# Optimization experiments

Hardware: AMD Instinct MI355X
Metric: run time of the kernel (lower is better)

The kernel has to match this reference:

```python
import itertools
import jax, jax.numpy as jnp
import numpy as np

N_LEVELS = 16
N_FEATS = 2
LOG2_T = 19
BASE_RES = 16.0
FINEST_RES = 512.0
N_POINTS = 2 ** 21
MASK = np.uint32((1 << LOG2_T) - 1)
PRIMES = jnp.array([1, 2654435761, 805459861], dtype=jnp.uint32)
# 8 corner offsets of a voxel, [8, 3]
OFFSETS = jnp.array(list(itertools.product([0, 1], repeat=3)), dtype=jnp.int32)
BOX_MIN = jnp.zeros((3,), dtype=jnp.float32)
BOX_MAX = jnp.ones((3,), dtype=jnp.float32)
# per-level growth factor b = exp((log(finest)-log(base))/(L-1))
B_FACTOR = float(np.exp((np.log(FINEST_RES) - np.log(BASE_RES)) / (N_LEVELS - 1)))


def setup_inputs() -> dict:
    key = jax.random.key(0)
    k1, k2 = jax.random.split(key)
    x = jax.random.uniform(k1, (N_POINTS, 3), dtype=jnp.float32)
    # nn.init.uniform_(w, a=-1e-4, b=1e-4)
    tables = jax.random.uniform(k2, (N_LEVELS, 2 ** LOG2_T, N_FEATS),
                                dtype=jnp.float32, minval=-1e-4, maxval=1e-4)
    return {"x": x, "tables": tables}


def _hash(vidx):
    # vidx: [N, 8, 3] int32 voxel-corner integer coords
    v = vidx.astype(jnp.uint32)
    h = (v[..., 0] * PRIMES[0]) ^ (v[..., 1] * PRIMES[1]) ^ (v[..., 2] * PRIMES[2])
    return (h & MASK).astype(jnp.int32)  # [N, 8]


def _embed_level(x, table, resolution):
    # x: [N,3] float, table: [T,F], resolution: python float
    grid = (BOX_MAX - BOX_MIN) / resolution                      # [3]
    xc = jnp.clip(x, BOX_MIN, BOX_MAX)
    bl = jnp.floor((xc - BOX_MIN) / grid).astype(jnp.int32)      # [N,3]
    vmin = bl.astype(jnp.float32) * grid + BOX_MIN               # [N,3]
    vidx = bl[:, None, :] + OFFSETS[None, :, :]                  # [N,8,3]
    emb = table[_hash(vidx)]                                     # [N,8,F]
    rel = (xc - vmin) / grid                                     # [N,3]
    # trilinear weights: prod over dims of rel (offset=1) / 1-rel (offset=0)
    w = jnp.prod(jnp.where(OFFSETS[None, :, :] == 1,
                           rel[:, None, :], 1.0 - rel[:, None, :]), axis=-1)  # [N,8]
    return jnp.sum(w[..., None] * emb, axis=1)                   # [N,F]


def reference(x, tables):
    outs = []
    for i in range(N_LEVELS):
        resolution = float(np.floor(BASE_RES * B_FACTOR ** i))
        outs.append(_embed_level(x, tables[i], resolution))
    return jnp.concatenate(outs, axis=-1)  # [N, L*F]
```

## Files before the change

### kernel.cpp

```cpp
#include <hip/hip_runtime.h>
#include <stdint.h>


constexpr int kLevels = 16;
constexpr int kPoints = 1 << 21;
constexpr uint32_t kTableSize = 1u << 19;
constexpr uint32_t kMask = kTableSize - 1u;
constexpr size_t kPackedBytes = (size_t)kLevels * kTableSize * 4;
constexpr size_t kLvlOutBytes = (size_t)kLevels * kPoints * 4;

typedef float f32x4 __attribute__((ext_vector_type(4)));
typedef uint32_t u32x4 __attribute__((ext_vector_type(4)));

constexpr int kS0 = 17, kS1 = 21, kS2 = 26;
constexpr int kN0 = kS0 * kS0 * kS0;
constexpr int kN1 = kS1 * kS1 * kS1;
constexpr int kN2 = kS2 * kS2 * kS2;
constexpr int kB1 = kN0, kB2 = kN0 + kN1;
constexpr int kNDense = kN0 + kN1 + kN2;

constexpr int kV3n = 33 * 33 * 33;
constexpr int kV4n = 41 * 41 * 41;
constexpr int kV5n = 51 * 51 * 51;
constexpr int kV6n = 65 * 65 * 65;
constexpr int kVTot = kV3n + kV4n + kV5n + kV6n;
constexpr size_t kV3Base = 131072;
constexpr size_t kV4Base = kV3Base + (size_t)kV3n * 32;
constexpr size_t kV5Base = kV4Base + (size_t)kV4n * 32;
constexpr size_t kV6Base = kPackedBytes + (size_t)7 * kPoints * 4;

__constant__ float c_res[kLevels] = {
    16.f, 20.f, 25.f, 32.f, 40.f, 50.f, 64.f, 80.f,
    101.f, 128.f, 161.f, 203.f, 256.f, 322.f, 406.f, 512.f};

__device__ __forceinline__ uint32_t bf16_rtne_hi(float f) {
    uint32_t u = __float_as_uint(f);
    return (u + 0x7FFFu + ((u >> 16) & 1u)) >> 16;
}
__device__ __forceinline__ float bflo(uint32_t e) {
    return __uint_as_float(e << 16);
}
__device__ __forceinline__ float bfhi(uint32_t e) {
    return __uint_as_float(e & 0xFFFF0000u);
}

__global__ __launch_bounds__(256) void pack_tables_kernel(
    const float* __restrict__ tables, uint32_t* __restrict__ packed, int base)
{
    const int i = base + blockIdx.x * 256 + threadIdx.x;
    const f32x4 v = reinterpret_cast<const f32x4*>(tables)[i];
    uint2 o;
    o.x = bf16_rtne_hi(v.x) | (bf16_rtne_hi(v.y) << 16);
    o.y = bf16_rtne_hi(v.z) | (bf16_rtne_hi(v.w) << 16);
    reinterpret_cast<uint2*>(packed)[i] = o;
}

template <int S, int LVL>
__device__ __forceinline__ void build_dense_one(
    int r, const float* __restrict__ tables, uint32_t* __restrict__ dst)
{
    const int bz = r % S;
    const int t = r / S;
    const int by = t % S;
    const int bx = t / S;
    const uint32_t h = ((uint32_t)bx ^ ((uint32_t)by * 2654435761u) ^
                        ((uint32_t)bz * 805459861u)) & kMask;
    const float* src = tables + (((size_t)LVL << 19) + h) * 2;
    dst[r] = bf16_rtne_hi(src[0]) | (bf16_rtne_hi(src[1]) << 16);
}

__global__ __launch_bounds__(256) void build_dense012_kernel(
    const float* __restrict__ tables, uint32_t* __restrict__ dense)
{
    const int idx = blockIdx.x * 256 + threadIdx.x;
    if (idx >= kNDense) return;
    if (idx < kB1)      build_dense_one<kS0, 0>(idx,       tables, dense);
    else if (idx < kB2) build_dense_one<kS1, 1>(idx - kB1, tables, dense + kB1);
    else                build_dense_one<kS2, 2>(idx - kB2, tables, dense + kB2);
}

template <int S, int LVL>
__device__ __forceinline__ void build_vox_one(
    int v, const float* __restrict__ tables, u32x4* __restrict__ dst)
{
    const int bz = v % S;
    const int t = v / S;
    const int by = t % S;
    const int bx = t / S;
    const float* tab = tables + (((size_t)LVL << 19) * 2);
    uint32_t e[8];
#pragma unroll
    for (int c = 0; c < 8; ++c) {
        const uint32_t xx = (uint32_t)(bx + ((c >> 2) & 1));
        const uint32_t yy = (uint32_t)(by + ((c >> 1) & 1));
        const uint32_t zz = (uint32_t)(bz + (c & 1));
        const uint32_t h = (xx ^ (yy * 2654435761u) ^ (zz * 805459861u)) & kMask;
        const float* src = tab + (size_t)h * 2;
        e[c] = bf16_rtne_hi(src[0]) | (bf16_rtne_hi(src[1]) << 16);
    }
    u32x4 q0, q1;
    q0.x = e[0]; q0.y = e[1]; q0.z = e[2]; q0.w = e[3];
    q1.x = e[4]; q1.y = e[5]; q1.z = e[6]; q1.w = e[7];
    dst[2 * v + 0] = q0;
    dst[2 * v + 1] = q1;
}

__global__ __launch_bounds__(256) void build_vox_kernel(
    const float* __restrict__ tables, char* __restrict__ ws)
{
    const int v = blockIdx.x * 256 + threadIdx.x;
    if (v >= kVTot) return;
    if (v < kV3n)
        build_vox_one<33, 3>(v, tables, (u32x4*)(ws + kV3Base));
    else if (v < kV3n + kV4n)
        build_vox_one<41, 4>(v - kV3n, tables, (u32x4*)(ws + kV4Base));
    else if (v < kV3n + kV4n + kV5n)
        build_vox_one<51, 5>(v - kV3n - kV4n, tables, (u32x4*)(ws + kV5Base));
    else
        build_vox_one<65, 6>(v - kV3n - kV4n - kV5n, tables,
                             (u32x4*)(ws + kV6Base));
}

template <int S, int BASE, int LVL>
__device__ __forceinline__ void eval_coarse(
    const uint32_t* __restrict__ lds, float px, float py, float pz, float r,
    uint32_t* __restrict__ lvl_out, int n)
{
    const float tx = px * r, ty = py * r, tz = pz * r;
    const float fx = floorf(tx), fy = floorf(ty), fz = floorf(tz);
    const int bx = (int)fx, by = (int)fy, bz = (int)fz;
    const float rx = tx - fx, ry = ty - fy, rz = tz - fz;
    const int c = BASE + (bx * S + by) * S + bz;
    const uint32_t e000 = lds[c],             e001 = lds[c + 1];
    const uint32_t e010 = lds[c + S],         e011 = lds[c + S + 1];
    const uint32_t e100 = lds[c + S * S],     e101 = lds[c + S * S + 1];
    const uint32_t e110 = lds[c + S * S + S], e111 = lds[c + S * S + S + 1];
    const float wx1 = rx, wx0 = 1.f - rx;
    const float wy1 = ry, wy0 = 1.f - ry;
    const float wz1 = rz, wz0 = 1.f - rz;
    float a0 = 0.f, a1 = 0.f;
    a0 = fmaf(wx0 * wy0 * wz0, bflo(e000), a0);
    a1 = fmaf(wx0 * wy0 * wz0, bfhi(e000), a1);
    a0 = fmaf(wx0 * wy0 * wz1, bflo(e001), a0);
    a1 = fmaf(wx0 * wy0 * wz1, bfhi(e001), a1);
    a0 = fmaf(wx0 * wy1 * wz0, bflo(e010), a0);
    a1 = fmaf(wx0 * wy1 * wz0, bfhi(e010), a1);
    a0 = fmaf(wx0 * wy1 * wz1, bflo(e011), a0);
    a1 = fmaf(wx0 * wy1 * wz1, bfhi(e011), a1);
    a0 = fmaf(wx1 * wy0 * wz0, bflo(e100), a0);
    a1 = fmaf(wx1 * wy0 * wz0, bfhi(e100), a1);
    a0 = fmaf(wx1 * wy0 * wz1, bflo(e101), a0);
    a1 = fmaf(wx1 * wy0 * wz1, bfhi(e101), a1);
    a0 = fmaf(wx1 * wy1 * wz0, bflo(e110), a0);
    a1 = fmaf(wx1 * wy1 * wz0, bfhi(e110), a1);
    a0 = fmaf(wx1 * wy1 * wz1, bflo(e111), a0);
    a1 = fmaf(wx1 * wy1 * wz1, bfhi(e111), a1);
    lvl_out[(size_t)LVL * kPoints + n] =
        bf16_rtne_hi(a0) | (bf16_rtne_hi(a1) << 16);
}

__global__ __launch_bounds__(512) void coarse_kernel(
    const float* __restrict__ x, const uint32_t* __restrict__ dense,
    uint32_t* __restrict__ lvl_out)
{
    __shared__ uint32_t s_tab[kNDense];
    for (int i = threadIdx.x; i < kNDense; i += 512) s_tab[i] = dense[i];
    __syncthreads();

    const int n0 = blockIdx.x * 2048 + threadIdx.x;
#pragma unroll
    for (int k = 0; k < 4; ++k) {
        const int n = n0 + k * 512;
        const float px = fminf(fmaxf(x[3 * n + 0], 0.0f), 1.0f);
        const float py = fminf(fmaxf(x[3 * n + 1], 0.0f), 1.0f);
        const float pz = fminf(fmaxf(x[3 * n + 2], 0.0f), 1.0f);
        eval_coarse<kS0, 0,   0>(s_tab, px, py, pz, 16.f, lvl_out, n);
        eval_coarse<kS1, kB1, 1>(s_tab, px, py, pz, 20.f, lvl_out, n);
        eval_coarse<kS2, kB2, 2>(s_tab, px, py, pz, 25.f, lvl_out, n);
    }
}

template <int R, int LVL>
__device__ __forceinline__ void eval_vox(
    const u32x4* __restrict__ V, float px, float py, float pz,
    uint32_t* __restrict__ lvl_out, int n)
{
    const float r = (float)R;
    const float tx = px * r, ty = py * r, tz = pz * r;
    const float fx = floorf(tx), fy = floorf(ty), fz = floorf(tz);
    const int bx = (int)fx, by = (int)fy, bz = (int)fz;
    const float rx = tx - fx, ry = ty - fy, rz = tz - fz;
    constexpr int S = R + 1;
    const int idx = (bx * S + by) * S + bz;
    const u32x4 q0 = V[2 * idx + 0];
    const u32x4 q1 = V[2 * idx + 1];
    const float wx1 = rx, wx0 = 1.f - rx;
    const float wy1 = ry, wy0 = 1.f - ry;
    const float wz1 = rz, wz0 = 1.f - rz;
    float a0 = 0.f, a1 = 0.f;
    a0 = fmaf(wx0 * wy0 * wz0, bflo(q0.x), a0);
    a1 = fmaf(wx0 * wy0 * wz0, bfhi(q0.x), a1);
    a0 = fmaf(wx0 * wy0 * wz1, bflo(q0.y), a0);
    a1 = fmaf(wx0 * wy0 * wz1, bfhi(q0.y), a1);
    a0 = fmaf(wx0 * wy1 * wz0, bflo(q0.z), a0);
    a1 = fmaf(wx0 * wy1 * wz0, bfhi(q0.z), a1);
    a0 = fmaf(wx0 * wy1 * wz1, bflo(q0.w), a0);
    a1 = fmaf(wx0 * wy1 * wz1, bfhi(q0.w), a1);
    a0 = fmaf(wx1 * wy0 * wz0, bflo(q1.x), a0);
    a1 = fmaf(wx1 * wy0 * wz0, bfhi(q1.x), a1);
    a0 = fmaf(wx1 * wy0 * wz1, bflo(q1.y), a0);
    a1 = fmaf(wx1 * wy0 * wz1, bfhi(q1.y), a1);
    a0 = fmaf(wx1 * wy1 * wz0, bflo(q1.z), a0);
    a1 = fmaf(wx1 * wy1 * wz0, bfhi(q1.z), a1);
    a0 = fmaf(wx1 * wy1 * wz1, bflo(q1.w), a0);
    a1 = fmaf(wx1 * wy1 * wz1, bfhi(q1.w), a1);
    lvl_out[(size_t)LVL * kPoints + n] =
        bf16_rtne_hi(a0) | (bf16_rtne_hi(a1) << 16);
}

__global__ __launch_bounds__(256) void mid_kernel(
    const float* __restrict__ x, const char* __restrict__ ws,
    uint32_t* __restrict__ lvl_out)
{
    const int b = blockIdx.x;
    const int sub = b >> 11;
    const int chunk = b & 2047;
    const int n0 = chunk * 1024 + threadIdx.x;
#pragma unroll
    for (int k = 0; k < 4; ++k) {
        const int n = n0 + k * 256;
        const float px = fminf(fmaxf(x[3 * n + 0], 0.0f), 1.0f);
        const float py = fminf(fmaxf(x[3 * n + 1], 0.0f), 1.0f);
        const float pz = fminf(fmaxf(x[3 * n + 2], 0.0f), 1.0f);
        if (sub == 0)
            eval_vox<32, 3>((const u32x4*)(ws + kV3Base), px, py, pz, lvl_out, n);
        else if (sub == 1)
            eval_vox<40, 4>((const u32x4*)(ws + kV4Base), px, py, pz, lvl_out, n);
        else if (sub == 2)
            eval_vox<50, 5>((const u32x4*)(ws + kV5Base), px, py, pz, lvl_out, n);
        else
            eval_vox<64, 6>((const u32x4*)(ws + kV6Base), px, py, pz, lvl_out, n);
    }
}

struct PtSt {
    float rx, ry, rz;
    uint32_t sel;
    uint2 p0, p1, p2, p3;
};

__device__ __forceinline__ void issue_pt(
    PtSt& st, const float* __restrict__ x, int n, float r,
    const uint32_t* __restrict__ tab)
{
    const float px = fminf(fmaxf(x[3 * n + 0], 0.f), 1.f);
    const float py = fminf(fmaxf(x[3 * n + 1], 0.f), 1.f);
    const float pz = fminf(fmaxf(x[3 * n + 2], 0.f), 1.f);
    const float tx = px * r, ty = py * r, tz = pz * r;
    const float fx = floorf(tx), fy = floorf(ty), fz = floorf(tz);
    const int bx = (int)fx, by = (int)fy, bz = (int)fz;
    st.rx = tx - fx;  st.ry = ty - fy;  st.rz = tz - fz;
    const uint32_t hy0 = (uint32_t)by * 2654435761u;
    const uint32_t hy1 = (uint32_t)(by + 1) * 2654435761u;
    const uint32_t hz0 = (uint32_t)bz * 805459861u;
    const uint32_t hz1 = (uint32_t)(bz + 1) * 805459861u;
    const uint32_t bxu = (uint32_t)bx, bx1 = bxu + 1u;
    const uint32_t m0 = hy0 ^ hz0, m1 = hy0 ^ hz1;
    const uint32_t m2 = hy1 ^ hz0, m3 = hy1 ^ hz1;
    if ((bx & 1) == 0) {
        const uint32_t h0 = (bxu ^ m0) & kMask;
        const uint32_t h1 = (bxu ^ m1) & kMask;
        const uint32_t h2 = (bxu ^ m2) & kMask;
        const uint32_t h3 = (bxu ^ m3) & kMask;
        st.sel = (h0 & 1u) | ((h1 & 1u) << 1) |
                 ((h2 & 1u) << 2) | ((h3 & 1u) << 3);
        st.p0 = *reinterpret_cast<const uint2*>(tab + (h0 & ~1u));
        st.p1 = *reinterpret_cast<const uint2*>(tab + (h1 & ~1u));
        st.p2 = *reinterpret_cast<const uint2*>(tab + (h2 & ~1u));
        st.p3 = *reinterpret_cast<const uint2*>(tab + (h3 & ~1u));
    } else {
        st.sel = 0u;
        st.p0.x = tab[(bxu ^ m0) & kMask];  st.p0.y = tab[(bx1 ^ m0) & kMask];
        st.p1.x = tab[(bxu ^ m1) & kMask];  st.p1.y = tab[(bx1 ^ m1) & kMask];
        st.p2.x = tab[(bxu ^ m2) & kMask];  st.p2.y = tab[(bx1 ^ m2) & kMask];
        st.p3.x = tab[(bxu ^ m3) & kMask];  st.p3.y = tab[(bx1 ^ m3) & kMask];
    }
}

__device__ __forceinline__ void consume_pt(
    const PtSt& st, uint32_t* __restrict__ w, int n)
{
    const float wx1 = st.rx, wx0 = 1.f - st.rx;
    const float wy1 = st.ry, wy0 = 1.f - st.ry;
    const float wz1 = st.rz, wz0 = 1.f - st.rz;
    const float w0 = wy0 * wz0, w1 = wy0 * wz1;
    const float w2 = wy1 * wz0, w3 = wy1 * wz1;
    const uint32_t e0 = (st.sel & 1u) ? st.p0.y : st.p0.x;
    const uint32_t f0 = (st.sel & 1u) ? st.p0.x : st.p0.y;
    const uint32_t e1 = (st.sel & 2u) ? st.p1.y : st.p1.x;
    const uint32_t f1 = (st.sel & 2u) ? st.p1.x : st.p1.y;
    const uint32_t e2 = (st.sel & 4u) ? st.p2.y : st.p2.x;
    const uint32_t f2 = (st.sel & 4u) ? st.p2.x : st.p2.y;
    const uint32_t e3 = (st.sel & 8u) ? st.p3.y : st.p3.x;
    const uint32_t f3 = (st.sel & 8u) ? st.p3.x : st.p3.y;
    float a0 = 0.f, a1 = 0.f;
    a0 = fmaf(w0, fmaf(wx0, bflo(e0), wx1 * bflo(f0)), a0);
    a1 = fmaf(w0, fmaf(wx0, bfhi(e0), wx1 * bfhi(f0)), a1);
    a0 = fmaf(w1, fmaf(wx0, bflo(e1), wx1 * bflo(f1)), a0);
    a1 = fmaf(w1, fmaf(wx0, bfhi(e1), wx1 * bfhi(f1)), a1);
    a0 = fmaf(w2, fmaf(wx0, bflo(e2), wx1 * bflo(f2)), a0);
    a1 = fmaf(w2, fmaf(wx0, bfhi(e2), wx1 * bfhi(f2)), a1);
    a0 = fmaf(w3, fmaf(wx0, bflo(e3), wx1 * bflo(f3)), a0);
    a1 = fmaf(w3, fmaf(wx0, bfhi(e3), wx1 * bfhi(f3)), a1);
    w[n] = bf16_rtne_hi(a0) | (bf16_rtne_hi(a1) << 16);
}

__global__ __launch_bounds__(256) void fine_kernel(
    const float* __restrict__ x,
    const uint32_t* __restrict__ packed,
    uint32_t* __restrict__ lvl_out)
{
    const int b = blockIdx.x;
    const int level = 7 + (b >> 11);
    const int chunk = b & 2047;

    const float r = c_res[level];
    const uint32_t* __restrict__ tab = packed + (size_t)level * kTableSize;
    uint32_t* __restrict__ w = lvl_out + (size_t)level * kPoints;

    const int n0 = chunk * 1024 + threadIdx.x;

    PtSt A, B;
    issue_pt(A, x, n0 + 0 * 256, r, tab);
    issue_pt(B, x, n0 + 1 * 256, r, tab);
    __builtin_amdgcn_sched_barrier(0);
    consume_pt(A, w, n0 + 0 * 256);
    __builtin_amdgcn_sched_barrier(0);
    issue_pt(A, x, n0 + 2 * 256, r, tab);
    __builtin_amdgcn_sched_barrier(0);
    consume_pt(B, w, n0 + 1 * 256);
    __builtin_amdgcn_sched_barrier(0);
    issue_pt(B, x, n0 + 3 * 256, r, tab);
    __builtin_amdgcn_sched_barrier(0);
    consume_pt(A, w, n0 + 2 * 256);
    __builtin_amdgcn_sched_barrier(0);
    consume_pt(B, w, n0 + 3 * 256);
}

__global__ __launch_bounds__(256) void untile_kernel(
    const uint32_t* __restrict__ lvl_out, float* __restrict__ out)
{
    const int n = blockIdx.x * 256 + threadIdx.x;
    float vals[2 * kLevels];
#pragma unroll
    for (int l = 0; l < kLevels; ++l) {
        const uint32_t u = lvl_out[(size_t)l * kPoints + n];
        vals[2 * l + 0] = bflo(u);
        vals[2 * l + 1] = bfhi(u);
    }
    float4* o4 = reinterpret_cast<float4*>(out + (size_t)n * (2 * kLevels));
#pragma unroll
    for (int kq = 0; kq < 8; ++kq) {
        o4[kq] = make_float4(vals[4 * kq + 0], vals[4 * kq + 1],
                             vals[4 * kq + 2], vals[4 * kq + 3]);
    }
}

__device__ __forceinline__ void eval_level(
    float px, float py, float pz, float r,
    const uint32_t* __restrict__ tab, float& a0, float& a1)
{
    const float tx = px * r, ty = py * r, tz = pz * r;
    const float fx = floorf(tx), fy = floorf(ty), fz = floorf(tz);
    const int bx = (int)fx, by = (int)fy, bz = (int)fz;
    const float rx = tx - fx, ry = ty - fy, rz = tz - fz;

    const uint32_t hx0 = (uint32_t)bx;
    const uint32_t hx1 = (uint32_t)(bx + 1);
    const uint32_t hy0 = (uint32_t)by * 2654435761u;
    const uint32_t hy1 = (uint32_t)(by + 1) * 2654435761u;
    const uint32_t hz0 = (uint32_t)bz * 805459861u;
    const uint32_t hz1 = (uint32_t)(bz + 1) * 805459861u;

    const float wx1 = rx, wx0 = 1.0f - rx;
    const float wy1 = ry, wy0 = 1.0f - ry;
    const float wz1 = rz, wz0 = 1.0f - rz;

    a0 = 0.0f; a1 = 0.0f;
#pragma unroll
    for (int c = 0; c < 8; ++c) {
        const uint32_t h = (((c & 4) ? hx1 : hx0) ^
                            ((c & 2) ? hy1 : hy0) ^
                            ((c & 1) ? hz1 : hz0)) & kMask;
        const uint32_t e = tab[h];
        const float w = ((c & 4) ? wx1 : wx0) *
                        ((c & 2) ? wy1 : wy0) *
                        ((c & 1) ? wz1 : wz0);
        a0 = fmaf(w, bflo(e), a0);
        a1 = fmaf(w, bfhi(e), a1);
    }
}

__global__ __launch_bounds__(256) void direct_kernel(
    const float* __restrict__ x,
    const float* __restrict__ tables,
    float* __restrict__ out)
{
    const int n = blockIdx.x * 256 + threadIdx.x;
    float px = fminf(fmaxf(x[3 * n + 0], 0.0f), 1.0f);
    float py = fminf(fmaxf(x[3 * n + 1], 0.0f), 1.0f);
    float pz = fminf(fmaxf(x[3 * n + 2], 0.0f), 1.0f);

    const float res_tab[kLevels] = {
        16.f, 20.f, 25.f, 32.f, 40.f, 50.f, 64.f, 80.f,
        101.f, 128.f, 161.f, 203.f, 256.f, 322.f, 406.f, 512.f};

    float acc[2 * kLevels];
#pragma unroll
    for (int l = 0; l < kLevels; ++l) {
        const float r = res_tab[l];
        const float tx = px * r, ty = py * r, tz = pz * r;
        const float fx = floorf(tx), fy = floorf(ty), fz = floorf(tz);
        const int bx = (int)fx, by = (int)fy, bz = (int)fz;
        const float rx = tx - fx, ry = ty - fy, rz = tz - fz;
        const uint32_t hx0 = (uint32_t)bx;
        const uint32_t hx1 = (uint32_t)(bx + 1);
        const uint32_t hy0 = (uint32_t)by * 2654435761u;
        const uint32_t hy1 = (uint32_t)(by + 1) * 2654435761u;
        const uint32_t hz0 = (uint32_t)bz * 805459861u;
        const uint32_t hz1 = (uint32_t)(bz + 1) * 805459861u;
        const float wx1 = rx, wx0 = 1.0f - rx;
        const float wy1 = ry, wy0 = 1.0f - ry;
        const float wz1 = rz, wz0 = 1.0f - rz;
        const float2* __restrict__ tab =
            reinterpret_cast<const float2*>(tables) + (size_t)l * kTableSize;
        float a0 = 0.0f, a1 = 0.0f;
#pragma unroll
        for (int c = 0; c < 8; ++c) {
            const uint32_t h = (((c & 4) ? hx1 : hx0) ^
                                ((c & 2) ? hy1 : hy0) ^
                                ((c & 1) ? hz1 : hz0)) & kMask;
            const float2 e = tab[h];
            const float w = ((c & 4) ? wx1 : wx0) *
                            ((c & 2) ? wy1 : wy0) *
                            ((c & 1) ? wz1 : wz0);
            a0 = fmaf(w, e.x, a0);
            a1 = fmaf(w, e.y, a1);
        }
        acc[2 * l + 0] = a0;
        acc[2 * l + 1] = a1;
    }
    float4* o4 = reinterpret_cast<float4*>(out + (size_t)n * (2 * kLevels));
#pragma unroll
    for (int kq = 0; kq < 8; ++kq) {
        o4[kq] = make_float4(acc[4 * kq + 0], acc[4 * kq + 1],
                             acc[4 * kq + 2], acc[4 * kq + 3]);
    }
}

__global__ __launch_bounds__(256) void direct_packed_kernel(
    const float* __restrict__ x,
    const uint32_t* __restrict__ packed,
    float* __restrict__ out)
{
    const int n = blockIdx.x * 256 + threadIdx.x;
    float px = fminf(fmaxf(x[3 * n + 0], 0.0f), 1.0f);
    float py = fminf(fmaxf(x[3 * n + 1], 0.0f), 1.0f);
    float pz = fminf(fmaxf(x[3 * n + 2], 0.0f), 1.0f);

    const float res_tab[kLevels] = {
        16.f, 20.f, 25.f, 32.f, 40.f, 50.f, 64.f, 80.f,
        101.f, 128.f, 161.f, 203.f, 256.f, 322.f, 406.f, 512.f};

    float acc[2 * kLevels];
#pragma unroll
    for (int l = 0; l < kLevels; ++l) {
        float a0, a1;
        eval_level(px, py, pz, res_tab[l],
                   packed + (size_t)l * kTableSize, a0, a1);
        acc[2 * l + 0] = a0;
        acc[2 * l + 1] = a1;
    }
    float4* o4 = reinterpret_cast<float4*>(out + (size_t)n * (2 * kLevels));
#pragma unroll
    for (int kq = 0; kq < 8; ++kq) {
        o4[kq] = make_float4(acc[4 * kq + 0], acc[4 * kq + 1],
                             acc[4 * kq + 2], acc[4 * kq + 3]);
    }
}

extern "C" void kernel_launch(void* const* d_in, const int* in_sizes, int n_in,
                              void* d_out, int out_size, void* d_ws, size_t ws_size,
                              hipStream_t stream) {
    const float* x = (const float*)d_in[0];
    const float* tables = (const float*)d_in[1];
    float* out = (float*)d_out;

    if (ws_size >= kPackedBytes + kLvlOutBytes) {
        char* ws = (char*)d_ws;
        uint32_t* packed = (uint32_t*)ws;
        uint32_t* lvl_out = (uint32_t*)(ws + kPackedBytes);
        uint32_t* dense012 = (uint32_t*)ws;

        hipLaunchKernelGGL(pack_tables_kernel,
                           dim3((9 << 19) / 2 / 256), dim3(256),
                           0, stream, tables, packed, (7 << 19) / 2);
        hipLaunchKernelGGL(build_dense012_kernel,
                           dim3((kNDense + 255) / 256), dim3(256),
                           0, stream, tables, dense012);
        hipLaunchKernelGGL(build_vox_kernel,
                           dim3((kVTot + 255) / 256), dim3(256),
                           0, stream, tables, ws);
        hipLaunchKernelGGL(coarse_kernel, dim3(kPoints / 2048), dim3(512),
                           0, stream, x, dense012, lvl_out);
        hipLaunchKernelGGL(mid_kernel, dim3(4 * 2048), dim3(256),
                           0, stream, x, (const char*)ws, lvl_out);
        hipLaunchKernelGGL(fine_kernel, dim3(9 * 2048), dim3(256),
                           0, stream, x, packed, lvl_out);
        hipLaunchKernelGGL(untile_kernel, dim3(kPoints / 256), dim3(256),
                           0, stream, lvl_out, out);
    } else if (ws_size >= kPackedBytes) {
        uint32_t* packed = (uint32_t*)d_ws;
        hipLaunchKernelGGL(pack_tables_kernel,
                           dim3((kLevels * kTableSize / 2) / 256), dim3(256),
                           0, stream, tables, packed, 0);
        hipLaunchKernelGGL(direct_packed_kernel, dim3(kPoints / 256), dim3(256),
                           0, stream, x, packed, out);
    } else {
        hipLaunchKernelGGL(direct_kernel, dim3(kPoints / 256), dim3(256),
                           0, stream, x, tables, out);
    }
}
```

Before: 562.1 us.

## Build per-vertex dense grids before voxel tables and software-pipeline mid levels

The voxel tables for levels 3-6 are now built in two steps. A new kernel first gathers one hashed bf16 entry per grid vertex into a dense array. The voxel builder then reads its 8 corners from that dense array instead of recomputing 8 hashes and doing 8 random gathers per voxel. The mid kernel is restructured to load all point coordinates up front and interleave two in-flight voxel loads with the math, using sched_barriers for double-buffering. This adds an extra kernel launch and workspace region at hard-coded offsets, and uses float2 loads in the dense builder.

```diff
diff --git a/kernel.cpp b/kernel.cpp
--- a/kernel.cpp
+++ b/kernel.cpp
@@ -28,6 +28,10 @@
 constexpr size_t kV4Base = kV3Base + (size_t)kV3n * 32;
 constexpr size_t kV5Base = kV4Base + (size_t)kV4n * 32;
 constexpr size_t kV6Base = kPackedBytes + (size_t)7 * kPoints * 4;
+constexpr size_t kD3Base = 7731456;
+constexpr size_t kD4Base = 7875328;
+constexpr size_t kD5Base = 8151296;
+constexpr size_t kD6Base = 8681984;
 
 __constant__ float c_res[kLevels] = {
     16.f, 20.f, 25.f, 32.f, 40.f, 50.f, 64.f, 80.f,
@@ -65,8 +69,9 @@
     const int bx = t / S;
     const uint32_t h = ((uint32_t)bx ^ ((uint32_t)by * 2654435761u) ^
                         ((uint32_t)bz * 805459861u)) & kMask;
-    const float* src = tables + (((size_t)LVL << 19) + h) * 2;
-    dst[r] = bf16_rtne_hi(src[0]) | (bf16_rtne_hi(src[1]) << 16);
+    const float2 src = *reinterpret_cast<const float2*>(
+        tables + (((size_t)LVL << 19) + h) * 2);
+    dst[r] = bf16_rtne_hi(src.x) | (bf16_rtne_hi(src.y) << 16);
 }
 
 __global__ __launch_bounds__(256) void build_dense012_kernel(
@@ -79,46 +84,64 @@
     else                build_dense_one<kS2, 2>(idx - kB2, tables, dense + kB2);
 }
 
-template <int S, int LVL>
+__global__ __launch_bounds__(256) void build_denseD_kernel(
+    const float* __restrict__ tables, char* __restrict__ ws)
+{
+    const int g = blockIdx.x * 256 + threadIdx.x;
+    if (g >= kVTot) return;
+    if (g < kV3n)
+        build_dense_one<33, 3>(g, tables, (uint32_t*)(ws + kD3Base));
+    else if (g < kV3n + kV4n)
+        build_dense_one<41, 4>(g - kV3n, tables, (uint32_t*)(ws + kD4Base));
+    else if (g < kV3n + kV4n + kV5n)
+        build_dense_one<51, 5>(g - kV3n - kV4n, tables,
+                               (uint32_t*)(ws + kD5Base));
+    else
+        build_dense_one<65, 6>(g - kV3n - kV4n - kV5n, tables,
+                               (uint32_t*)(ws + kD6Base));
+}
+
+template <int S>
 __device__ __forceinline__ void build_vox_one(
-    int v, const float* __restrict__ tables, u32x4* __restrict__ dst)
+    int v, const uint32_t* __restrict__ D, u32x4* __restrict__ dst)
 {
     const int bz = v % S;
     const int t = v / S;
     const int by = t % S;
     const int bx = t / S;
-    const float* tab = tables + (((size_t)LVL << 19) * 2);
-    uint32_t e[8];
-#pragma unroll
-    for (int c = 0; c < 8; ++c) {
-        const uint32_t xx = (uint32_t)(bx + ((c >> 2) & 1));
-        const uint32_t yy = (uint32_t)(by + ((c >> 1) & 1));
-        const uint32_t zz = (uint32_t)(bz + (c & 1));
-        const uint32_t h = (xx ^ (yy * 2654435761u) ^ (zz * 805459861u)) & kMask;
-        const float* src = tab + (size_t)h * 2;
-        e[c] = bf16_rtne_hi(src[0]) | (bf16_rtne_hi(src[1]) << 16);
-    }
+    const int x1 = (bx + 1 < S) ? bx + 1 : S - 1;
+    const int y1 = (by + 1 < S) ? by + 1 : S - 1;
+    const int z1 = (bz + 1 < S) ? bz + 1 : S - 1;
     u32x4 q0, q1;
-    q0.x = e[0]; q0.y = e[1]; q0.z = e[2]; q0.w = e[3];
-    q1.x = e[4]; q1.y = e[5]; q1.z = e[6]; q1.w = e[7];
+    q0.x = D[(bx * S + by) * S + bz];
+    q0.y = D[(bx * S + by) * S + z1];
+    q0.z = D[(bx * S + y1) * S + bz];
+    q0.w = D[(bx * S + y1) * S + z1];
+    q1.x = D[(x1 * S + by) * S + bz];
+    q1.y = D[(x1 * S + by) * S + z1];
+    q1.z = D[(x1 * S + y1) * S + bz];
+    q1.w = D[(x1 * S + y1) * S + z1];
     dst[2 * v + 0] = q0;
     dst[2 * v + 1] = q1;
 }
 
-__global__ __launch_bounds__(256) void build_vox_kernel(
-    const float* __restrict__ tables, char* __restrict__ ws)
+__global__ __launch_bounds__(256) void build_vox_kernel(char* __restrict__ ws)
 {
     const int v = blockIdx.x * 256 + threadIdx.x;
     if (v >= kVTot) return;
     if (v < kV3n)
-        build_vox_one<33, 3>(v, tables, (u32x4*)(ws + kV3Base));
+        build_vox_one<33>(v, (const uint32_t*)(ws + kD3Base),
+                          (u32x4*)(ws + kV3Base));
     else if (v < kV3n + kV4n)
-        build_vox_one<41, 4>(v - kV3n, tables, (u32x4*)(ws + kV4Base));
+        build_vox_one<41>(v - kV3n, (const uint32_t*)(ws + kD4Base),
+                          (u32x4*)(ws + kV4Base));
     else if (v < kV3n + kV4n + kV5n)
-        build_vox_one<51, 5>(v - kV3n - kV4n, tables, (u32x4*)(ws + kV5Base));
+        build_vox_one<51>(v - kV3n - kV4n, (const uint32_t*)(ws + kD5Base),
+                          (u32x4*)(ws + kV5Base));
     else
-        build_vox_one<65, 6>(v - kV3n - kV4n - kV5n, tables,
-                             (u32x4*)(ws + kV6Base));
+        build_vox_one<65>(v - kV3n - kV4n - kV5n,
+                          (const uint32_t*)(ws + kD6Base),
+                          (u32x4*)(ws + kV6Base));
 }
 
 template <int S, int BASE, int LVL>
@@ -180,42 +203,87 @@
     }
 }
 
-template <int R, int LVL>
-__device__ __forceinline__ void eval_vox(
-    const u32x4* __restrict__ V, float px, float py, float pz,
-    uint32_t* __restrict__ lvl_out, int n)
+struct MidSt {
+    float rx, ry, rz;
+    u32x4 q0, q1;
+};
+
+template <int R>
+__device__ __forceinline__ void issue_mid(
+    MidSt& st, const u32x4* __restrict__ V, float px, float py, float pz)
 {
     const float r = (float)R;
     const float tx = px * r, ty = py * r, tz = pz * r;
     const float fx = floorf(tx), fy = floorf(ty), fz = floorf(tz);
     const int bx = (int)fx, by = (int)fy, bz = (int)fz;
-    const float rx = tx - fx, ry = ty - fy, rz = tz - fz;
+    st.rx = tx - fx;  st.ry = ty - fy;  st.rz = tz - fz;
     constexpr int S = R + 1;
     const int idx = (bx * S + by) * S + bz;
-    const u32x4 q0 = V[2 * idx + 0];
-    const u32x4 q1 = V[2 * idx + 1];
-    const float wx1 = rx, wx0 = 1.f - rx;
-    const float wy1 = ry, wy0 = 1.f - ry;
-    const float wz1 = rz, wz0 = 1.f - rz;
+    st.q0 = V[2 * idx + 0];
+    st.q1 = V[2 * idx + 1];
+}
+
+__device__ __forceinline__ void consume_mid(
+    const MidSt& st, uint32_t* __restrict__ dst)
+{
+    const float wx1 = st.rx, wx0 = 1.f - st.rx;
+    const float wy1 = st.ry, wy0 = 1.f - st.ry;
+    const float wz1 = st.rz, wz0 = 1.f - st.rz;
     float a0 = 0.f, a1 = 0.f;
-    a0 = fmaf(wx0 * wy0 * wz0, bflo(q0.x), a0);
-    a1 = fmaf(wx0 * wy0 * wz0, bfhi(q0.x), a1);
-    a0 = fmaf(wx0 * wy0 * wz1, bflo(q0.y), a0);
-    a1 = fmaf(wx0 * wy0 * wz1, bfhi(q0.y), a1);
-    a0 = fmaf(wx0 * wy1 * wz0, bflo(q0.z), a0);
-    a1 = fmaf(wx0 * wy1 * wz0, bfhi(q0.z), a1);
-    a0 = fmaf(wx0 * wy1 * wz1, bflo(q0.w), a0);
-    a1 = fmaf(wx0 * wy1 * wz1, bfhi(q0.w), a1);
-    a0 = fmaf(wx1 * wy0 * wz0, bflo(q1.x), a0);
-    a1 = fmaf(wx1 * wy0 * wz0, bfhi(q1.x), a1);
-    a0 = fmaf(wx1 * wy0 * wz1, bflo(q1.y), a0);
-    a1 = fmaf(wx1 * wy0 * wz1, bfhi(q1.y), a1);
-    a0 = fmaf(wx1 * wy1 * wz0, bflo(q1.z), a0);
-    a1 = fmaf(wx1 * wy1 * wz0, bfhi(q1.z), a1);
-    a0 = fmaf(wx1 * wy1 * wz1, bflo(q1.w), a0);
-    a1 = fmaf(wx1 * wy1 * wz1, bfhi(q1.w), a1);
-    lvl_out[(size_t)LVL * kPoints + n] =
-        bf16_rtne_hi(a0) | (bf16_rtne_hi(a1) << 16);
+    a0 = fmaf(wx0 * wy0 * wz0, bflo(st.q0.x), a0);
+    a1 = fmaf(wx0 * wy0 * wz0, bfhi(st.q0.x), a1);
+    a0 = fmaf(wx0 * wy0 * wz1, bflo(st.q0.y), a0);
+    a1 = fmaf(wx0 * wy0 * wz1, bfhi(st.q0.y), a1);
+    a0 = fmaf(wx0 * wy1 * wz0, bflo(st.q0.z), a0);
+    a1 = fmaf(wx0 * wy1 * wz0, bfhi(st.q0.z), a1);
+    a0 = fmaf(wx0 * wy1 * wz1, bflo(st.q0.w), a0);
+    a1 = fmaf(wx0 * wy1 * wz1, bfhi(st.q0.w), a1);
+    a0 = fmaf(wx1 * wy0 * wz0, bflo(st.q1.x), a0);
+    a1 = fmaf(wx1 * wy0 * wz0, bfhi(st.q1.x), a1);
+    a0 = fmaf(wx1 * wy0 * wz1, bflo(st.q1.y), a0);
+    a1 = fmaf(wx1 * wy0 * wz1, bfhi(st.q1.y), a1);
+    a0 = fmaf(wx1 * wy1 * wz0, bflo(st.q1.z), a0);
+    a1 = fmaf(wx1 * wy1 * wz0, bfhi(st.q1.z), a1);
+    a0 = fmaf(wx1 * wy1 * wz1, bflo(st.q1.w), a0);
+    a1 = fmaf(wx1 * wy1 * wz1, bfhi(st.q1.w), a1);
+    *dst = bf16_rtne_hi(a0) | (bf16_rtne_hi(a1) << 16);
+}
+
+template <int R, int LVL>
+__device__ __forceinline__ void mid_level(
+    const float* __restrict__ x, const u32x4* __restrict__ V,
+    uint32_t* __restrict__ lvl_out, int n0)
+{
+    uint32_t* __restrict__ w = lvl_out + (size_t)LVL * kPoints;
+    const float px0 = fminf(fmaxf(x[3 * (n0 + 0 * 256) + 0], 0.f), 1.f);
+    const float py0 = fminf(fmaxf(x[3 * (n0 + 0 * 256) + 1], 0.f), 1.f);
+    const float pz0 = fminf(fmaxf(x[3 * (n0 + 0 * 256) + 2], 0.f), 1.f);
+    const float px1 = fminf(fmaxf(x[3 * (n0 + 1 * 256) + 0], 0.f), 1.f);
+    const float py1 = fminf(fmaxf(x[3 * (n0 + 1 * 256) + 1], 0.f), 1.f);
+    const float pz1 = fminf(fmaxf(x[3 * (n0 + 1 * 256) + 2], 0.f), 1.f);
+    const float px2 = fminf(fmaxf(x[3 * (n0 + 2 * 256) + 0], 0.f), 1.f);
+    const float py2 = fminf(fmaxf(x[3 * (n0 + 2 * 256) + 1], 0.f), 1.f);
+    const float pz2 = fminf(fmaxf(x[3 * (n0 + 2 * 256) + 2], 0.f), 1.f);
+    const float px3 = fminf(fmaxf(x[3 * (n0 + 3 * 256) + 0], 0.f), 1.f);
+    const float py3 = fminf(fmaxf(x[3 * (n0 + 3 * 256) + 1], 0.f), 1.f);
+    const float pz3 = fminf(fmaxf(x[3 * (n0 + 3 * 256) + 2], 0.f), 1.f);
+    __builtin_amdgcn_sched_barrier(0);
+
+    MidSt A, B;
+    issue_mid<R>(A, V, px0, py0, pz0);
+    issue_mid<R>(B, V, px1, py1, pz1);
+    __builtin_amdgcn_sched_barrier(0);
+    consume_mid(A, &w[n0 + 0 * 256]);
+    __builtin_amdgcn_sched_barrier(0);
+    issue_mid<R>(A, V, px2, py2, pz2);
+    __builtin_amdgcn_sched_barrier(0);
+    consume_mid(B, &w[n0 + 1 * 256]);
+    __builtin_amdgcn_sched_barrier(0);
+    issue_mid<R>(B, V, px3, py3, pz3);
+    __builtin_amdgcn_sched_barrier(0);
+    consume_mid(A, &w[n0 + 2 * 256]);
+    __builtin_amdgcn_sched_barrier(0);
+    consume_mid(B, &w[n0 + 3 * 256]);
 }
 
 __global__ __launch_bounds__(256) void mid_kernel(
@@ -226,21 +294,14 @@
     const int sub = b >> 11;
     const int chunk = b & 2047;
     const int n0 = chunk * 1024 + threadIdx.x;
-#pragma unroll
-    for (int k = 0; k < 4; ++k) {
-        const int n = n0 + k * 256;
-        const float px = fminf(fmaxf(x[3 * n + 0], 0.0f), 1.0f);
-        const float py = fminf(fmaxf(x[3 * n + 1], 0.0f), 1.0f);
-        const float pz = fminf(fmaxf(x[3 * n + 2], 0.0f), 1.0f);
-        if (sub == 0)
-            eval_vox<32, 3>((const u32x4*)(ws + kV3Base), px, py, pz, lvl_out, n);
-        else if (sub == 1)
-            eval_vox<40, 4>((const u32x4*)(ws + kV4Base), px, py, pz, lvl_out, n);
-        else if (sub == 2)
-            eval_vox<50, 5>((const u32x4*)(ws + kV5Base), px, py, pz, lvl_out, n);
-        else
-            eval_vox<64, 6>((const u32x4*)(ws + kV6Base), px, py, pz, lvl_out, n);
-    }
+    if (sub == 0)
+        mid_level<32, 3>(x, (const u32x4*)(ws + kV3Base), lvl_out, n0);
+    else if (sub == 1)
+        mid_level<40, 4>(x, (const u32x4*)(ws + kV4Base), lvl_out, n0);
+    else if (sub == 2)
+        mid_level<50, 5>(x, (const u32x4*)(ws + kV5Base), lvl_out, n0);
+    else
+        mid_level<64, 6>(x, (const u32x4*)(ws + kV6Base), lvl_out, n0);
 }
 
 struct PtSt {
@@ -508,9 +569,12 @@
         hipLaunchKernelGGL(build_dense012_kernel,
                            dim3((kNDense + 255) / 256), dim3(256),
                            0, stream, tables, dense012);
+        hipLaunchKernelGGL(build_denseD_kernel,
+                           dim3((kVTot + 255) / 256), dim3(256),
+                           0, stream, tables, ws);
         hipLaunchKernelGGL(build_vox_kernel,
                            dim3((kVTot + 255) / 256), dim3(256),
-                           0, stream, tables, ws);
+                           0, stream, ws);
         hipLaunchKernelGGL(coarse_kernel, dim3(kPoints / 2048), dim3(512),
                            0, stream, x, dense012, lvl_out);
         hipLaunchKernelGGL(mid_kernel, dim3(4 * 2048), dim3(256),
```

Result: no change. 557.0 us (median of 2 runs) (-0.9%).
